# Kernel tuning notes

Hardware: AMD Instinct MI355X
Metric: run time of the kernel (lower is better)

The kernel has to match this reference:

```python
import jax, jax.numpy as jnp
import numpy as np

B, S = 512, 256
NUM_LOC, NUM_USERS, D = 50000, 10000, 256
MAX_RECENT = 5
DQ = D // 4            # user/hour/weekday embed dim
TEMP = 3 * DQ          # temporal feature size
H2 = D // 2            # scorer hidden
NEG = -1e9


def setup_inputs() -> dict:
    key = jax.random.key(0)
    ks = jax.random.split(key, 25)
    p = lambda i, shape: jax.random.normal(ks[i], shape, jnp.float32) * 0.02

    locations = jax.random.randint(ks[0], (B, S), 0, NUM_LOC)
    users = jax.random.randint(ks[1], (B, S), 0, NUM_USERS)
    weekdays = jax.random.randint(ks[2], (B, S), 0, 8)
    start_mins = jax.random.randint(ks[3], (B, S), 0, 1440)
    lengths = jax.random.randint(ks[4], (B,), 1, S + 1)  # ragged valid lengths
    mask = jnp.arange(S)[None, :] < lengths[:, None]     # (B,S) bool prefix mask

    return {
        "locations": locations, "users": users, "weekdays": weekdays,
        "start_mins": start_mins, "mask": mask,
        # embedding tables (padding_idx=0 row zeroed, matching torch init)
        "loc_table": p(5, (NUM_LOC, D)).at[0].set(0.0),
        "user_table": p(6, (NUM_USERS, DQ)).at[0].set(0.0),
        "hour_table": p(7, (25, DQ)).at[0].set(0.0),
        "wd_table": p(8, (8, DQ)).at[0].set(0.0),
        # LSTM (PyTorch layout: gates i,f,g,o stacked)
        "W_ih": p(9, (4 * D, D + TEMP)), "W_hh": p(10, (4 * D, D)),
        "b_ih": p(11, (4 * D,)), "b_hh": p(12, (4 * D,)),
        # recent-location scorer MLP
        "sc_W1": p(13, (H2, D + 2)), "sc_b1": p(14, (H2,)),
        "sc_W2": p(15, (1, H2)), "sc_b2": p(16, (1,)),
        # new-location predictor MLP (dropout is identity in eval)
        "np_W1": p(17, (D, D)), "np_b1": p(18, (D,)),
        "np_W2": p(19, (NUM_LOC, D)), "np_b2": p(20, (NUM_LOC,)),
        # mix predictor
        "mx_W": p(21, (1, D)), "mx_b": p(22, (1,)),
    }


def _forward(locations, users, weekdays, start_mins, mask,
             loc_table, user_table, hour_table, wd_table,
             W_ih, W_hh, b_ih, b_hh,
             sc_W1, sc_b1, sc_W2, sc_b2,
             np_W1, np_b1, np_W2, np_b2, mx_W, mx_b):
    gelu = lambda x: jax.nn.gelu(x, approximate=False)  # torch nn.GELU default

    hours = jnp.clip(start_mins // 60, 0, 24)
    temporal = jnp.concatenate(
        [user_table[users], hour_table[hours], wd_table[weekdays]], axis=-1)
    x = jnp.concatenate([loc_table[locations], temporal], axis=-1)  # (B,S,D+TEMP)

    # --- LSTM over time via scan (PyTorch gate order i,f,g,o) ---
    def step(carry, xt):
        h, c = carry
        g = xt @ W_ih.T + b_ih + h @ W_hh.T + b_hh
        i, f, gg, o = jnp.split(g, 4, axis=-1)
        c = jax.nn.sigmoid(f) * c + jax.nn.sigmoid(i) * jnp.tanh(gg)
        h = jax.nn.sigmoid(o) * jnp.tanh(c)
        return (h, c), h

    h0 = jnp.zeros((x.shape[0], D), x.dtype)
    _, outs = jax.lax.scan(step, (h0, h0), jnp.swapaxes(x, 0, 1))
    output = jnp.swapaxes(outs, 0, 1)  # (B,S,D)

    seq_lens = mask.sum(axis=1).astype(jnp.int32) - 1  # last valid index
    bids = jnp.arange(output.shape[0])
    context = output[bids, seq_lens]                   # (B,D)

    # --- vectorized ragged recent-location scoring (j=0 is last visit) ---
    j = jnp.arange(MAX_RECENT)
    idx = seq_lens[:, None] - j[None, :]               # (B,R) indices from end
    valid = idx >= 0                                   # j < seq_len_b
    idxc = jnp.clip(idx, 0, S - 1)
    bidx = bids[:, None]
    rlocs = locations[bidx, idxc]                      # (B,R)
    rtimes = start_mins[bidx, idxc]
    cur_time = start_mins[bids, seq_lens][:, None]
    tdiff = ((cur_time - rtimes).astype(jnp.float32) / 1440.0)[..., None]
    pos = jnp.broadcast_to(j.astype(jnp.float32), rlocs.shape)[..., None]
    feats = jnp.concatenate([loc_table[rlocs], tdiff, pos], axis=-1)  # (B,R,D+2)
    scores = (gelu(feats @ sc_W1.T + sc_b1) @ sc_W2.T + sc_b2)[..., 0]  # (B,R)

    # drop entry jj if some newer valid entry j' < jj has the same location.
    eq = rlocs[:, :, None] == rlocs[:, None, :]        # (B, jj, j')
    newer = (j[:, None] > j[None, :])[None]            # jj > j'
    dup = jnp.any(eq & newer & valid[:, None, :], axis=-1)
    keep = valid & ~dup
    scatter_locs = jnp.where(keep, rlocs, NUM_LOC)     # out-of-range -> dropped

    recent_logits = jnp.full((rlocs.shape[0], NUM_LOC), NEG, jnp.float32)
    recent_logits = recent_logits.at[bidx, scatter_locs].set(scores, mode='drop')

    new_logits = gelu(context @ np_W1.T + np_b1) @ np_W2.T + np_b2  # (B,NUM_LOC)
    mix = jax.nn.sigmoid(context @ mx_W.T + mx_b) * 0.9 + 0.05     # (B,1)
    return mix * recent_logits + (1.0 - mix) * new_logits


def reference(locations, users, weekdays, start_mins, mask,
              loc_table, user_table, hour_table, wd_table,
              W_ih, W_hh, b_ih, b_hh,
              sc_W1, sc_b1, sc_W2, sc_b2,
              np_W1, np_b1, np_W2, np_b2, mx_W, mx_b):
    return _forward(locations, users, weekdays, start_mins, mask,
                    loc_table, user_table, hour_table, wd_table,
                    W_ih, W_hh, b_ih, b_hh,
                    sc_W1, sc_b1, sc_W2, sc_b2,
                    np_W1, np_b1, np_W2, np_b2, mx_W, mx_b)
```

## Files before the change

### kernel.cpp

```cpp
#include <hip/hip_runtime.h>
#include <hip/hip_bf16.h>
#include <math.h>

#define B_ 512
#define S_ 256
#define D_ 256
#define NLOC 50000
#define KX 448
#define G4 1024
#define NEGV -1000000000.0f

typedef __attribute__((ext_vector_type(8))) short short8;
typedef __attribute__((ext_vector_type(4))) float f32x4;

__device__ __forceinline__ float sigmoidf_(float x){ return 1.0f/(1.0f+expf(-x)); }
__device__ __forceinline__ float geluf_(float x){ return 0.5f*x*(1.0f+erff(x*0.70710678118654752f)); }
__device__ __forceinline__ unsigned short f2bf_(float x){
  __hip_bfloat16 h = __float2bfloat16(x);
  return *(unsigned short*)&h;
}
__device__ __forceinline__ float bf2f_(unsigned short u){
  __hip_bfloat16 h = *(__hip_bfloat16*)&u;
  return __bfloat162float(h);
}
__device__ __forceinline__ float fsig_(float x){
  return __fdividef(1.0f, 1.0f + __expf(-x));
}
__device__ __forceinline__ float ftanh2_(float x){
  float ax = fabsf(x);
  float x2 = x*x;
  float tp = x*(1.0f + x2*(-0.3333333333f + x2*(0.1333333333f + x2*(-0.05396825397f))));
  float e  = __expf(2.0f*fminf(ax, 15.0f));
  float te = 1.0f - __fdividef(2.0f, e + 1.0f);
  te = copysignf(te, x);
  return ax < 0.25f ? tp : te;
}
__device__ __forceinline__ void gld_lds16_(const unsigned short* gsrc, unsigned short* ldst){
  __builtin_amdgcn_global_load_lds((const __attribute__((address_space(1))) void*)gsrc,
                                   (__attribute__((address_space(3))) void*)ldst, 16, 0, 0);
}

__global__ void k_init(int* flag){
  if (blockIdx.x==0 && threadIdx.x==0) *flag = 0;
}

__global__ void k_detect(const unsigned char* m, int* flag){
  int i = blockIdx.x*256 + threadIdx.x;
  if ((i & 1) && i < B_*S_ && m[i]) atomicOr(flag, 1);
}

__global__ void k_seqlen(const void* mp, const int* flag, int* slens){
  int b = blockIdx.x*256 + threadIdx.x;
  if (b >= B_) return;
  int cnt = 0;
  if (*flag){
    const unsigned char* m = (const unsigned char*)mp;
    for (int s=0;s<S_;s++) cnt += (m[b*S_+s] != 0);
  } else {
    const int* m = (const int*)mp;
    for (int s=0;s<S_;s++) cnt += (m[b*S_+s] != 0);
  }
  slens[b] = cnt - 1;
}

__global__ void k_buildw(const float* wih, const float* bih, const float* bhh,
                         unsigned short* Wihbf, float* btot){
  int i = blockIdx.x*256 + threadIdx.x;
  if (i < G4*KX) Wihbf[i] = f2bf_(wih[i]);
  if (i < G4) btot[i] = bih[i] + bhh[i];
}

__global__ void k_packw(const float* __restrict__ whh, unsigned short* __restrict__ Whw){
  int idx = blockIdx.x*256 + threadIdx.x;
  if (idx >= 32768) return;
  int lane = idx & 63, f = (idx>>6)&7, kt = (idx>>9)&7, w = idx>>12;
  int q = f>>1, nt = f&1, l16 = lane&15, quad = lane>>4;
  int row = q*256 + w*32 + nt*16 + l16;
  int col = kt*32 + quad*8;
  const float* s = whh + (size_t)row*256 + col;
  short8 pk;
  #pragma unroll
  for (int e=0;e<8;e++) pk[e] = f2bf_(s[e]);
  *(short8*)(Whw + (size_t)idx*8) = pk;
}

__global__ __launch_bounds__(256) void k_gx(
    const int* __restrict__ loc, const int* __restrict__ usr,
    const int* __restrict__ wdy, const int* __restrict__ sm,
    const float* __restrict__ loct, const float* __restrict__ usert,
    const float* __restrict__ hourt, const float* __restrict__ wdt,
    const unsigned short* __restrict__ Wihbf, const float* __restrict__ btot,
    unsigned short* __restrict__ Gx){
  __shared__ unsigned short As[128][40];
  int tid = threadIdx.x;
  int n0 = blockIdx.x*128, m0 = blockIdx.y*128;
  int w = tid>>6, lane = tid&63;
  int quad = lane>>4, l16 = lane&15;
  int mw = (w>>1)*64, nw = (w&1)*64;
  f32x4 acc[4][4] = {};
  int r0 = tid>>2, seg = tid&3;
  for (int kt=0; kt<14; kt++){
    int k0 = kt*32;
    int kc = k0 + seg*8;
    #pragma unroll
    for (int rr=0; rr<2; rr++){
      int r = r0 + rr*64;
      int row = m0 + r;
      const float* src;
      if (kc < 256)      src = loct  + (size_t)loc[row]*256 + kc;
      else if (kc < 320) src = usert + (size_t)usr[row]*64 + (kc-256);
      else if (kc < 384) { int s = sm[row]; int hh = s/60; if (hh>24) hh=24; if (hh<0) hh=0;
                           src = hourt + (size_t)hh*64 + (kc-320); }
      else               src = wdt   + (size_t)wdy[row]*64 + (kc-384);
      float4 v0 = *(const float4*)(src);
      float4 v1 = *(const float4*)(src+4);
      short8 pk;
      pk[0]=f2bf_(v0.x); pk[1]=f2bf_(v0.y); pk[2]=f2bf_(v0.z); pk[3]=f2bf_(v0.w);
      pk[4]=f2bf_(v1.x); pk[5]=f2bf_(v1.y); pk[6]=f2bf_(v1.z); pk[7]=f2bf_(v1.w);
      *(short8*)&As[r][seg*8] = pk;
    }
    __syncthreads();
    short8 bfrag[4], afrag[4];
    #pragma unroll
    for (int nt=0; nt<4; nt++)
      bfrag[nt] = *(const short8*)(Wihbf + (size_t)(n0+nw+nt*16+l16)*KX + k0 + quad*8);
    #pragma unroll
    for (int mt=0; mt<4; mt++)
      afrag[mt] = *(const short8*)&As[mw+mt*16+l16][quad*8];
    #pragma unroll
    for (int mt=0; mt<4; mt++)
      #pragma unroll
      for (int nt=0; nt<4; nt++)
        acc[mt][nt] = __builtin_amdgcn_mfma_f32_16x16x32_bf16(afrag[mt], bfrag[nt], acc[mt][nt], 0, 0, 0);
    __syncthreads();
  }
  #pragma unroll
  for (int nt=0; nt<4; nt++){
    int col = n0 + nw + nt*16 + l16;
    float bv = btot[col];
    #pragma unroll
    for (int mt=0; mt<4; mt++){
      #pragma unroll
      for (int i=0; i<4; i++){
        int row = m0 + mw + mt*16 + quad*4 + i;
        int bb = row >> 8, tt = row & 255;
        Gx[((size_t)tt*B_ + bb)*G4 + col] = f2bf_(acc[mt][nt][i] + bv);
      }
    }
  }
}

__global__ __launch_bounds__(512, 2) void k_lstm(
    const unsigned short* __restrict__ Gx,
    const unsigned short* __restrict__ Whw,
    float* __restrict__ ctx, const int* __restrict__ slens){
  __shared__ unsigned short h_s[16][256];
  __shared__ unsigned short gx_s[16*1024];
  __shared__ unsigned short whhl[8][12][512];
  int tid = threadIdx.x;
  int w = tid >> 6, lane = tid & 63;
  int quad = lane >> 4, l16 = lane & 15;
  int b0 = blockIdx.x * 16;
  int dw = w * 32;

  for (int i = tid; i < 16*256; i += 512) ((unsigned short*)h_s)[i] = 0;

  #pragma unroll
  for (int c=0; c<12; c++)
    gld_lds16_(Whw + ((size_t)(w*64 + c))*512 + lane*8, &whhl[w][c][0]);

  float cst[2][4] = {{0.f,0.f,0.f,0.f},{0.f,0.f,0.f,0.f}};
  int slq[4];
  #pragma unroll
  for (int i=0;i<4;i++) slq[i] = slens[b0 + quad*4 + i];

  asm volatile("s_waitcnt vmcnt(0) lgkmcnt(0)" ::: "memory");
  __syncthreads();

  for (int t=0; t<S_; t++){
    {
      const unsigned short* src = Gx + ((size_t)t*B_ + b0)*G4 + w*2048 + lane*8;
      #pragma unroll
      for (int j=0;j<4;j++) gld_lds16_(src + j*512, &gx_s[w*2048 + j*512]);
    }
    unsigned long long wpa = (unsigned long long)Whw;
    asm volatile("" : "+s"(wpa));
    const unsigned short* sb = (const unsigned short*)wpa + ((size_t)(w*64))*512 + lane*8;

    short8 sA[13], sB[13], sC[13], sD[13];
    #pragma unroll
    for (int j=0;j<13;j++) sA[j] = *(const short8*)(sb + (size_t)(12+j)*512);
    #pragma unroll
    for (int j=0;j<13;j++) sB[j] = *(const short8*)(sb + (size_t)(25+j)*512);
    __builtin_amdgcn_sched_barrier(0);

    short8 af[8];
    #pragma unroll
    for (int kt=0;kt<8;kt++)
      af[kt] = *(const short8*)((const char*)h_s + l16*512 + ((((kt<<2)|quad) ^ (l16&7))<<4));
    f32x4 acc[4][2] = {};
    #pragma unroll
    for (int c=0;c<12;c++)
      acc[(c&7)>>1][c&1] = __builtin_amdgcn_mfma_f32_16x16x32_bf16(
          af[c>>3], *(const short8*)&whhl[w][c][lane*8], acc[(c&7)>>1][c&1], 0, 0, 0);
    __builtin_amdgcn_sched_barrier(0);

    #pragma unroll
    for (int j=0;j<13;j++){ int c = 12+j;
      acc[(c&7)>>1][c&1] = __builtin_amdgcn_mfma_f32_16x16x32_bf16(
          af[c>>3], sA[j], acc[(c&7)>>1][c&1], 0, 0, 0); }
    __builtin_amdgcn_sched_barrier(0);

    #pragma unroll
    for (int j=0;j<13;j++) sC[j] = *(const short8*)(sb + (size_t)(38+j)*512);
    #pragma unroll
    for (int j=0;j<13;j++){ int c = 25+j;
      acc[(c&7)>>1][c&1] = __builtin_amdgcn_mfma_f32_16x16x32_bf16(
          af[c>>3], sB[j], acc[(c&7)>>1][c&1], 0, 0, 0); }
    __builtin_amdgcn_sched_barrier(0);

    #pragma unroll
    for (int j=0;j<13;j++) sD[j] = *(const short8*)(sb + (size_t)(51+j)*512);
    #pragma unroll
    for (int j=0;j<13;j++){ int c = 38+j;
      acc[(c&7)>>1][c&1] = __builtin_amdgcn_mfma_f32_16x16x32_bf16(
          af[c>>3], sC[j], acc[(c&7)>>1][c&1], 0, 0, 0); }
    __builtin_amdgcn_sched_barrier(0);

    #pragma unroll
    for (int j=0;j<13;j++){ int c = 51+j;
      acc[(c&7)>>1][c&1] = __builtin_amdgcn_mfma_f32_16x16x32_bf16(
          af[c>>3], sD[j], acc[(c&7)>>1][c&1], 0, 0, 0); }

    asm volatile("s_waitcnt vmcnt(0) lgkmcnt(0)" ::: "memory");
    __builtin_amdgcn_sched_barrier(0);
    __builtin_amdgcn_s_barrier();

    const unsigned int* gxw = (const unsigned int*)&gx_s[0];
    int half = l16 & 1;
    #pragma unroll
    for (int nt=0;nt<2;nt++){
      int d = dw + nt*16 + l16;
      int dbase2 = (dw + nt*16) >> 1;
      int chunkx = d >> 3;
      #pragma unroll
      for (int i=0;i<4;i++){
        int r = quad*4 + i;
        int base = r*512 + dbase2 + (l16>>1);
        unsigned int u0 = gxw[base];
        unsigned int u1 = gxw[base + 128];
        unsigned int u2 = gxw[base + 256];
        unsigned int u3 = gxw[base + 384];
        unsigned short s0 = half ? (unsigned short)(u0>>16) : (unsigned short)(u0&0xffff);
        unsigned short s1 = half ? (unsigned short)(u1>>16) : (unsigned short)(u1&0xffff);
        unsigned short s2 = half ? (unsigned short)(u2>>16) : (unsigned short)(u2&0xffff);
        unsigned short s3 = half ? (unsigned short)(u3>>16) : (unsigned short)(u3&0xffff);
        float gi = acc[0][nt][i] + bf2f_(s0);
        float gf = acc[1][nt][i] + bf2f_(s1);
        float gg = acc[2][nt][i] + bf2f_(s2);
        float go = acc[3][nt][i] + bf2f_(s3);
        float cn = fsig_(gf)*cst[nt][i] + fsig_(gi)*ftanh2_(gg);
        float hn = fsig_(go)*ftanh2_(cn);
        cst[nt][i] = cn;
        *(unsigned short*)((char*)h_s + r*512 + ((chunkx ^ (r&7))<<4) + (d&7)*2) = f2bf_(hn);
        if (t == slq[i]) ctx[(size_t)(b0 + r)*D_ + d] = hn;
      }
    }

    asm volatile("s_waitcnt lgkmcnt(0)" ::: "memory");
    __builtin_amdgcn_sched_barrier(0);
    __builtin_amdgcn_s_barrier();
  }
}

__global__ void k_post1(const float* __restrict__ ctx, const float* __restrict__ W1,
                        const float* __restrict__ b1, const float* __restrict__ mxW,
                        const float* __restrict__ mxb, float* newhid, float* mixv){
  __shared__ float cs[256];
  __shared__ float red[256];
  int b = blockIdx.x, tid = threadIdx.x;
  cs[tid] = ctx[(size_t)b*D_ + tid];
  __syncthreads();
  float a = b1[tid];
  const float* wr = W1 + (size_t)tid*D_;
  for (int k=0; k<D_; k++) a += cs[k]*wr[k];
  newhid[(size_t)b*D_ + tid] = geluf_(a);
  red[tid] = cs[tid]*mxW[tid];
  __syncthreads();
  for (int s=128; s>0; s>>=1){ if (tid<s) red[tid]+=red[tid+s]; __syncthreads(); }
  if (tid==0) mixv[b] = sigmoidf_(red[0]+mxb[0])*0.9f + 0.05f;
}

__global__ void k_recent(const int* __restrict__ loc, const int* __restrict__ sm,
                         const int* __restrict__ slens, const float* __restrict__ loct,
                         const float* __restrict__ W1, const float* __restrict__ b1,
                         const float* __restrict__ W2, const float* __restrict__ b2,
                         float* scores, int* rlocs, int* keep){
  __shared__ int rl[5], vs[5];
  __shared__ float td[5];
  __shared__ float red[128];
  int b = blockIdx.x, tid = threadIdx.x;
  int sl = slens[b];
  if (tid < 5){
    int idx = sl - tid;
    int v = idx >= 0;
    int ic = v ? idx : 0;
    rl[tid] = loc[b*S_ + ic];
    vs[tid] = v;
    int cur = sm[b*S_ + sl];
    td[tid] = (float)(cur - sm[b*S_ + ic]) * (1.0f/1440.0f);
  }
  __syncthreads();
  for (int j=0; j<5; j++){
    const float* lrow = loct + (size_t)rl[j]*D_;
    const float* wr = W1 + (size_t)tid*258;
    float a = b1[tid];
    for (int k=0; k<D_; k++) a += lrow[k]*wr[k];
    a += td[j]*wr[256] + (float)j*wr[257];
    red[tid] = geluf_(a)*W2[tid];
    __syncthreads();
    for (int s=64; s>0; s>>=1){ if (tid<s) red[tid]+=red[tid+s]; __syncthreads(); }
    if (tid==0) scores[b*5+j] = red[0] + b2[0];
    __syncthreads();
  }
  if (tid==0){
    for (int j=0; j<5; j++){
      int dup = 0;
      for (int k=0; k<j; k++) dup |= (rl[j]==rl[k]) && vs[k];
      keep[b*5+j] = vs[j] && !dup;
      rlocs[b*5+j] = rl[j];
    }
  }
}

__global__ __launch_bounds__(256) void k_final(const float* __restrict__ newhid,
    const float* __restrict__ W2, const float* __restrict__ b2,
    const float* __restrict__ mixv, float* __restrict__ out){
  __shared__ float Hs[16][260];
  __shared__ float Wl[64][65];
  int tid = threadIdx.x;
  int l0 = blockIdx.x*64, b0 = blockIdx.y*16;
  int ll = tid & 63, bq = tid >> 6;
  #pragma unroll
  for (int r=0; r<16; r++) Hs[r][tid] = newhid[(size_t)(b0+r)*D_ + tid];
  float acc[4] = {0.f,0.f,0.f,0.f};
  for (int kt=0; kt<4; kt++){
    int k0 = kt*64;
    __syncthreads();
    #pragma unroll
    for (int r=0; r<4; r++){
      int row = 4*r + bq;
      int l = l0 + row;
      Wl[row][ll] = (l < NLOC) ? W2[(size_t)l*D_ + k0 + ll] : 0.f;
    }
    __syncthreads();
    #pragma unroll
    for (int kk=0; kk<64; kk++){
      float wv = Wl[ll][kk];
      #pragma unroll
      for (int bi=0; bi<4; bi++) acc[bi] += wv * Hs[bq*4+bi][k0+kk];
    }
  }
  int l = l0 + ll;
  if (l < NLOC){
    float bias = b2[l];
    #pragma unroll
    for (int bi=0; bi<4; bi++){
      int b = b0 + bq*4 + bi;
      float mx = mixv[b];
      out[(size_t)b*NLOC + l] = mx*NEGV + (1.0f-mx)*(acc[bi] + bias);
    }
  }
}

__global__ void k_scatter(const float* __restrict__ newhid, const float* __restrict__ W2,
                          const float* __restrict__ b2, const float* __restrict__ mixv,
                          const float* __restrict__ scores, const int* __restrict__ rlocs,
                          const int* __restrict__ keep, float* out){
  int b = blockIdx.x, lane = threadIdx.x;
  float mx = mixv[b];
  for (int j=0; j<5; j++){
    if (!keep[b*5+j]) continue;
    int rl = rlocs[b*5+j];
    const float* wr = W2 + (size_t)rl*D_;
    const float* hr = newhid + (size_t)b*D_;
    float a = 0.f;
    #pragma unroll
    for (int q=0; q<4; q++){ int k = lane + 64*q; a += hr[k]*wr[k]; }
    #pragma unroll
    for (int off=32; off>0; off>>=1) a += __shfl_xor(a, off, 64);
    if (lane==0)
      out[(size_t)b*NLOC + rl] = mx*scores[b*5+j] + (1.0f-mx)*(a + b2[rl]);
  }
}

extern "C" void kernel_launch(void* const* d_in, const int* in_sizes, int n_in,
                              void* d_out, int out_size, void* d_ws, size_t ws_size,
                              hipStream_t stream){
  const int* locations   = (const int*)d_in[0];
  const int* users       = (const int*)d_in[1];
  const int* weekdays    = (const int*)d_in[2];
  const int* start_mins  = (const int*)d_in[3];
  const void* mask       = d_in[4];
  const float* loc_table = (const float*)d_in[5];
  const float* user_table= (const float*)d_in[6];
  const float* hour_table= (const float*)d_in[7];
  const float* wd_table  = (const float*)d_in[8];
  const float* W_ih      = (const float*)d_in[9];
  const float* W_hh      = (const float*)d_in[10];
  const float* b_ih      = (const float*)d_in[11];
  const float* b_hh      = (const float*)d_in[12];
  const float* sc_W1     = (const float*)d_in[13];
  const float* sc_b1     = (const float*)d_in[14];
  const float* sc_W2     = (const float*)d_in[15];
  const float* sc_b2     = (const float*)d_in[16];
  const float* np_W1     = (const float*)d_in[17];
  const float* np_b1     = (const float*)d_in[18];
  const float* np_W2     = (const float*)d_in[19];
  const float* np_b2     = (const float*)d_in[20];
  const float* mx_W      = (const float*)d_in[21];
  const float* mx_b      = (const float*)d_in[22];
  float* out = (float*)d_out;

  char* w = (char*)d_ws;
  size_t o = 0;
  auto alloc = [&](size_t bytes)->void*{ void* p = w + o; o += (bytes + 255) & ~(size_t)255; return p; };
  unsigned short* Gx    = (unsigned short*)alloc((size_t)B_*S_*G4*sizeof(short));
  unsigned short* Wihbf = (unsigned short*)alloc((size_t)G4*KX*sizeof(short));
  unsigned short* Whw   = (unsigned short*)alloc((size_t)G4*D_*sizeof(short));
  float* btot   = (float*)alloc((size_t)G4*sizeof(float));
  float* ctx    = (float*)alloc((size_t)B_*D_*sizeof(float));
  float* newhid = (float*)alloc((size_t)B_*D_*sizeof(float));
  float* mixv   = (float*)alloc((size_t)B_*sizeof(float));
  float* scores = (float*)alloc((size_t)B_*5*sizeof(float));
  int*   slens  = (int*)alloc((size_t)B_*sizeof(int));
  int*   rlocs  = (int*)alloc((size_t)B_*5*sizeof(int));
  int*   keep   = (int*)alloc((size_t)B_*5*sizeof(int));
  int*   flag   = (int*)alloc(sizeof(int));

  k_init<<<1, 64, 0, stream>>>(flag);
  k_detect<<<512, 256, 0, stream>>>((const unsigned char*)mask, flag);
  k_seqlen<<<2, 256, 0, stream>>>(mask, flag, slens);
  k_buildw<<<1792, 256, 0, stream>>>(W_ih, b_ih, b_hh, Wihbf, btot);
  k_packw<<<128, 256, 0, stream>>>(W_hh, Whw);
  k_gx<<<dim3(8,1024), 256, 0, stream>>>(locations, users, weekdays, start_mins,
                                         loc_table, user_table, hour_table, wd_table,
                                         Wihbf, btot, Gx);
  k_lstm<<<32, 512, 0, stream>>>(Gx, Whw, ctx, slens);
  k_post1<<<512, 256, 0, stream>>>(ctx, np_W1, np_b1, mx_W, mx_b, newhid, mixv);
  k_recent<<<512, 128, 0, stream>>>(locations, start_mins, slens, loc_table,
                                    sc_W1, sc_b1, sc_W2, sc_b2, scores, rlocs, keep);
  k_final<<<dim3(782,32), 256, 0, stream>>>(newhid, np_W2, np_b2, mixv, out);
  k_scatter<<<512, 64, 0, stream>>>(newhid, np_W2, np_b2, mixv, scores, rlocs, keep, out);
}
```

Baseline: 3.067 ms.

## Stream LSTM recurrent weights through a 4-slot LDS ring buffer

The per-step W_hh chunks that were loaded from global memory into registers in four batches of 13 are now streamed one chunk at a time into a 4-slot LDS ring buffer using async global-to-LDS loads, with explicit vmcnt waits. The number of LDS-resident chunks drops from 12 to 8 to make room for the ring. The aim is to cut register pressure and overlap weight loads with MFMA work. The trade-off is that prefetch depth is only three chunks per wave, so each step may stall on load latency 56 times in sequence. The vmcnt waits also count the in-flight Gx loads, which may force them to finish earlier than before.

After: 3.128 ms. 1.02x slower.

```diff
diff --git a/kernel.cpp b/kernel.cpp
--- a/kernel.cpp
+++ b/kernel.cpp
@@ -156,7 +156,8 @@
     float* __restrict__ ctx, const int* __restrict__ slens){
   __shared__ unsigned short h_s[16][256];
   __shared__ unsigned short gx_s[16*1024];
-  __shared__ unsigned short whhl[8][12][512];
+  __shared__ unsigned short whhl[8][8][512];
+  __shared__ unsigned short whr[8][4][512];
   int tid = threadIdx.x;
   int w = tid >> 6, lane = tid & 63;
   int quad = lane >> 4, l16 = lane & 15;
@@ -166,7 +167,7 @@
   for (int i = tid; i < 16*256; i += 512) ((unsigned short*)h_s)[i] = 0;
 
   #pragma unroll
-  for (int c=0; c<12; c++)
+  for (int c=0; c<8; c++)
     gld_lds16_(Whw + ((size_t)(w*64 + c))*512 + lane*8, &whhl[w][c][0]);
 
   float cst[2][4] = {{0.f,0.f,0.f,0.f},{0.f,0.f,0.f,0.f}};
@@ -176,6 +177,8 @@
 
   asm volatile("s_waitcnt vmcnt(0) lgkmcnt(0)" ::: "memory");
   __syncthreads();
+
+  const unsigned short* sb = Whw + ((size_t)(w*64 + 8))*512 + lane*8;
 
   for (int t=0; t<S_; t++){
     {
@@ -183,15 +186,8 @@
       #pragma unroll
       for (int j=0;j<4;j++) gld_lds16_(src + j*512, &gx_s[w*2048 + j*512]);
     }
-    unsigned long long wpa = (unsigned long long)Whw;
-    asm volatile("" : "+s"(wpa));
-    const unsigned short* sb = (const unsigned short*)wpa + ((size_t)(w*64))*512 + lane*8;
-
-    short8 sA[13], sB[13], sC[13], sD[13];
-    #pragma unroll
-    for (int j=0;j<13;j++) sA[j] = *(const short8*)(sb + (size_t)(12+j)*512);
-    #pragma unroll
-    for (int j=0;j<13;j++) sB[j] = *(const short8*)(sb + (size_t)(25+j)*512);
+    #pragma unroll
+    for (int j=0;j<3;j++) gld_lds16_(sb + (size_t)j*512, &whr[w][j][0]);
     __builtin_amdgcn_sched_barrier(0);
 
     short8 af[8];
@@ -200,37 +196,24 @@
       af[kt] = *(const short8*)((const char*)h_s + l16*512 + ((((kt<<2)|quad) ^ (l16&7))<<4));
     f32x4 acc[4][2] = {};
     #pragma unroll
-    for (int c=0;c<12;c++)
+    for (int f=0;f<8;f++)
+      acc[f>>1][f&1] = __builtin_amdgcn_mfma_f32_16x16x32_bf16(
+          af[0], *(const short8*)&whhl[w][f][lane*8], acc[f>>1][f&1], 0, 0, 0);
+    __builtin_amdgcn_sched_barrier(0);
+
+    #pragma unroll
+    for (int i=0;i<56;i++){
+      if (i+3 < 56) gld_lds16_(sb + (size_t)(i+3)*512, &whr[w][(i+3)&3][0]);
+      if (i <= 52)      asm volatile("s_waitcnt vmcnt(3)" ::: "memory");
+      else if (i == 53) asm volatile("s_waitcnt vmcnt(2)" ::: "memory");
+      else if (i == 54) asm volatile("s_waitcnt vmcnt(1)" ::: "memory");
+      else              asm volatile("s_waitcnt vmcnt(0)" ::: "memory");
+      __builtin_amdgcn_sched_barrier(0);
+      short8 bb = *(const short8*)&whr[w][i&3][lane*8];
+      int c = 8+i;
       acc[(c&7)>>1][c&1] = __builtin_amdgcn_mfma_f32_16x16x32_bf16(
-          af[c>>3], *(const short8*)&whhl[w][c][lane*8], acc[(c&7)>>1][c&1], 0, 0, 0);
-    __builtin_amdgcn_sched_barrier(0);
-
-    #pragma unroll
-    for (int j=0;j<13;j++){ int c = 12+j;
-      acc[(c&7)>>1][c&1] = __builtin_amdgcn_mfma_f32_16x16x32_bf16(
-          af[c>>3], sA[j], acc[(c&7)>>1][c&1], 0, 0, 0); }
-    __builtin_amdgcn_sched_barrier(0);
-
-    #pragma unroll
-    for (int j=0;j<13;j++) sC[j] = *(const short8*)(sb + (size_t)(38+j)*512);
-    #pragma unroll
-    for (int j=0;j<13;j++){ int c = 25+j;
-      acc[(c&7)>>1][c&1] = __builtin_amdgcn_mfma_f32_16x16x32_bf16(
-          af[c>>3], sB[j], acc[(c&7)>>1][c&1], 0, 0, 0); }
-    __builtin_amdgcn_sched_barrier(0);
-
-    #pragma unroll
-    for (int j=0;j<13;j++) sD[j] = *(const short8*)(sb + (size_t)(51+j)*512);
-    #pragma unroll
-    for (int j=0;j<13;j++){ int c = 38+j;
-      acc[(c&7)>>1][c&1] = __builtin_amdgcn_mfma_f32_16x16x32_bf16(
-          af[c>>3], sC[j], acc[(c&7)>>1][c&1], 0, 0, 0); }
-    __builtin_amdgcn_sched_barrier(0);
-
-    #pragma unroll
-    for (int j=0;j<13;j++){ int c = 51+j;
-      acc[(c&7)>>1][c&1] = __builtin_amdgcn_mfma_f32_16x16x32_bf16(
-          af[c>>3], sD[j], acc[(c&7)>>1][c&1], 0, 0, 0); }
+          af[c>>3], bb, acc[(c&7)>>1][c&1], 0, 0, 0);
+    }
 
     asm volatile("s_waitcnt vmcnt(0) lgkmcnt(0)" ::: "memory");
     __builtin_amdgcn_sched_barrier(0);
```
